# Optimization experiments

Measured on AMD Instinct MI355X. Metric: run time of the kernel, lower is better.

## Reference

```python
import jax, jax.numpy as jnp
import numpy as np

NBINS = (128, 64, 32)
MIN_BIN_WIDTH = 1e-3
MIN_BIN_HEIGHT = 1e-3


def quadratic_spline(inputs, unnorm_widths, unnorm_heights):
    """Piecewise-quadratic CDF spline (nflows-style). inputs: (N,) in [0,1],
    unnorm_widths: (N, nb), unnorm_heights: (N, nb+1). Returns (outputs, logabsdet)."""
    num_bins = unnorm_widths.shape[-1]
    widths = jax.nn.softmax(unnorm_widths, axis=-1)
    widths = MIN_BIN_WIDTH + (1.0 - MIN_BIN_WIDTH * num_bins) * widths
    hexp = jnp.exp(unnorm_heights)
    # normalize piecewise-linear pdf to integrate to 1
    area = jnp.sum(0.5 * (hexp[:, :-1] + hexp[:, 1:]) * widths, axis=-1, keepdims=True)
    heights = hexp / area
    heights = MIN_BIN_HEIGHT + (1.0 - MIN_BIN_HEIGHT) * heights
    bin_cdf = jnp.cumsum(0.5 * (heights[:, :-1] + heights[:, 1:]) * widths, axis=-1)
    bin_left_cdf = jnp.pad(bin_cdf.at[:, -1].set(1.0), ((0, 0), (1, 0)))
    bin_loc = jnp.cumsum(widths, axis=-1)
    bin_locations = jnp.pad(bin_loc.at[:, -1].set(1.0), ((0, 0), (1, 0)))
    bin_idx = jnp.clip(jnp.sum((inputs[:, None] >= bin_locations).astype(jnp.int32), axis=-1) - 1,
                       0, num_bins - 1)[:, None]
    take = lambda t, i: jnp.take_along_axis(t, i, axis=-1)[:, 0]
    loc = take(bin_locations, bin_idx)
    w = take(widths, bin_idx)
    cdf = take(bin_left_cdf, bin_idx)
    hl = take(heights, bin_idx)
    hr = take(heights, bin_idx + 1)
    alpha = (inputs - loc) / w
    outputs = jnp.clip(0.5 * (hr - hl) * w * alpha * alpha + hl * w * alpha + cdf, 0.0, 1.0)
    logabsdet = jnp.log(alpha * (hr - hl) + hl)
    return outputs, logabsdet


def _forward(coordinates, clustering, delta_height_weight, delta_baseline_weight,
             unnormalized_heights, unnormalized_widths, baseline_bias,
             genes_oi, local_gene_ix, local_cellxgene_ix, localcellxgene_ix):
    n_total_genes = delta_baseline_weight.shape[0]
    # decoder
    dhw = delta_height_weight[genes_oi]                            # (G, L, K)
    mixture_delta = jnp.einsum('cl,glk->cgk', clustering, dhw)     # (C, G, K)
    baseline_delta = clustering @ delta_baseline_weight.T          # (C, n_total)
    baseline = jax.nn.softmax(jnp.log(baseline_bias)[None, :] + baseline_delta, axis=-1)
    baseline_cuts = baseline.reshape(-1)[localcellxgene_ix]        # (N,)
    delta = mixture_delta.reshape(-1, mixture_delta.shape[-1])[local_cellxgene_ix]  # (N, K)
    gene_global = genes_oi[local_gene_ix]                          # (N,)
    # quadratic spline stack log_prob (base = Uniform[0,1])
    x = coordinates
    logabsdet = jnp.zeros_like(coordinates)
    ho = 0
    wo = 0
    for n in NBINS:
        uh = unnormalized_heights[:, ho:ho + n][gene_global] + delta[:, ho:ho + n]
        uw = unnormalized_widths[:, wo:wo + n - 1][gene_global]
        x, lad = quadratic_spline(x, uw, uh)
        logabsdet = logabsdet + lad
        ho += n
        wo += n - 1
    likelihood_position = logabsdet
    likelihood_region = jnp.log(baseline_cuts) + jnp.log(jnp.asarray(n_total_genes, jnp.float32))
    elbo = -(likelihood_position + likelihood_region).sum()
    # KL regularization (scales = exp(log 1.0) = 1)
    half_log_2pi = float(0.5 * np.log(2.0 * np.pi))
    mixture_kl = -0.5 * dhw * dhw - half_log_2pi
    baseline_kl = -0.5 * jnp.square(delta_baseline_weight[genes_oi]) - half_log_2pi
    return elbo - mixture_kl.sum() - baseline_kl.sum()


def setup_inputs() -> dict:
    key = jax.random.key(0)
    ks = jax.random.split(key, 10)
    N, C, G, NT, L = 500_000, 1000, 500, 10_000, 16
    K = sum(NBINS)                # 224 heights / delta components
    W = sum(n - 1 for n in NBINS)  # 221 widths
    coordinates = jax.random.uniform(ks[0], (N,), jnp.float32, 1e-4, 1.0 - 1e-4)
    cluster_id = jax.random.randint(ks[1], (C,), 0, L)
    clustering = jax.nn.one_hot(cluster_id, L, dtype=jnp.float32)
    genes_oi = jnp.sort(jax.random.permutation(ks[2], NT)[:G]).astype(jnp.int32)
    cell_ix = jax.random.randint(ks[3], (N,), 0, C)
    local_gene_ix = jax.random.randint(ks[4], (N,), 0, G).astype(jnp.int32)
    local_cellxgene_ix = (cell_ix * G + local_gene_ix).astype(jnp.int32)
    localcellxgene_ix = (cell_ix * NT + genes_oi[local_gene_ix]).astype(jnp.int32)
    delta_height_weight = jax.random.normal(ks[5], (NT, L, K), jnp.float32) * 0.05
    delta_baseline_weight = jax.random.uniform(ks[6], (NT, L), jnp.float32, -0.25, 0.25)
    unnormalized_heights = jax.random.normal(ks[7], (NT, K), jnp.float32) * 0.1
    unnormalized_widths = jax.random.normal(ks[8], (NT, W), jnp.float32) * 0.1
    baseline_bias = jax.random.uniform(ks[9], (NT,), jnp.float32, 1e-5, 1.0)
    return {
        'coordinates': coordinates, 'clustering': clustering,
        'delta_height_weight': delta_height_weight,
        'delta_baseline_weight': delta_baseline_weight,
        'unnormalized_heights': unnormalized_heights,
        'unnormalized_widths': unnormalized_widths,
        'baseline_bias': baseline_bias,
        'genes_oi': genes_oi, 'local_gene_ix': local_gene_ix,
        'local_cellxgene_ix': local_cellxgene_ix,
        'localcellxgene_ix': localcellxgene_ix,
    }


def reference(coordinates, clustering, delta_height_weight, delta_baseline_weight,
              unnormalized_heights, unnormalized_widths, baseline_bias,
              genes_oi, local_gene_ix, local_cellxgene_ix, localcellxgene_ix):
    return _forward(coordinates, clustering, delta_height_weight, delta_baseline_weight,
                    unnormalized_heights, unnormalized_widths, baseline_bias,
                    genes_oi, local_gene_ix, local_cellxgene_ix, localcellxgene_ix)
```

## Files before the change

kernel.cpp:

```cpp
#include <hip/hip_runtime.h>
#include <math.h>


#define CAP 192
static constexpr float  F_MBW = 1e-3f;
static constexpr float  F_MBH = 1e-3f;
static constexpr double D_HL2PI = 0.918938533204672741780329736406;


__global__ void __launch_bounds__(256)
kA(const float* __restrict__ clustering, int* __restrict__ cid,
   double* __restrict__ dpart, int* __restrict__ cnt, int C, int L, int P) {
  int bid = blockIdx.x, tid = threadIdx.x;
  if (bid < 4) {
    int c = bid * 256 + tid;
    if (c < C) {
      const float* row = clustering + (size_t)c * L;
      int best = 0; float bv = row[0];
      for (int l = 1; l < L; ++l) { float v = row[l]; if (v > bv) { bv = v; best = l; } }
      cid[c] = best;
    }
  } else {
    if (bid == 4 && tid < 128) dpart[tid] = 0.0;
    int i = (bid - 4) * 256 + tid;
    if (i < P) cnt[i] = 0;
  }
}

__global__ void __launch_bounds__(256)
kB(const float* __restrict__ coords, const int* __restrict__ lgi,
   const int* __restrict__ lcg, const int* __restrict__ cid,
   const float* __restrict__ bb, const float* __restrict__ dbw,
   int* __restrict__ cnt, float* __restrict__ xs, double* __restrict__ dpart,
   int N, int G, int L, int NT, int SCAT) {
  int bid = blockIdx.x;
  if (bid < SCAT) {
    int n0 = (bid * 256 + threadIdx.x) * 2;
    #pragma unroll
    for (int q = 0; q < 2; ++q) {
      int n = n0 + q;
      if (n < N) {
        int pair = lgi[n] * L + cid[lcg[n] / G];
        int pos = atomicAdd(&cnt[pair], 1);
        if (pos < CAP) xs[(size_t)pair * CAP + pos] = coords[n];
      }
    }
  } else {
    int g = (bid - SCAT) * 256 + threadIdx.x;
    float s[16];
    #pragma unroll
    for (int l = 0; l < 16; ++l) s[l] = 0.f;
    if (g < NT) {
      float b = bb[g];
      const float4* row = (const float4*)(dbw + (size_t)g * 16);
      #pragma unroll
      for (int q = 0; q < 4; ++q) {
        float4 v = row[q];
        s[4 * q + 0] = b * expf(v.x); s[4 * q + 1] = b * expf(v.y);
        s[4 * q + 2] = b * expf(v.z); s[4 * q + 3] = b * expf(v.w);
      }
    }
    __shared__ float partl[4][16];
    int lane = threadIdx.x & 63, wv = threadIdx.x >> 6;
    #pragma unroll
    for (int l = 0; l < 16; ++l) {
      float v = s[l];
      for (int off = 32; off; off >>= 1) v += __shfl_xor(v, off);
      if (lane == 0) partl[wv][l] = v;
    }
    __syncthreads();
    if (threadIdx.x < 16) {
      float t = partl[0][threadIdx.x] + partl[1][threadIdx.x]
              + partl[2][threadIdx.x] + partl[3][threadIdx.x];
      atomicAdd(&dpart[threadIdx.x * 8], (double)t);
    }
  }
}

static __device__ __forceinline__ float wscan(float v, int lane) {
  #pragma unroll
  for (int off = 1; off < 64; off <<= 1) {
    float u = __shfl_up(v, off, 64);
    if (lane >= off) v += u;
  }
  return v;
}

__global__ void __launch_bounds__(64)
k_pair(const float* __restrict__ uh, const float* __restrict__ uw,
       const float* __restrict__ dhw, const int* __restrict__ genes_oi,
       const float* __restrict__ xs, const int* __restrict__ cnt,
       const float* __restrict__ bb, const float* __restrict__ dbw,
       const double* __restrict__ dpart,
       float* __restrict__ partA, float* __restrict__ partB,
       int L, int K, int W, int NT) {
  int p = blockIdx.x;
  int g = p / L;
  int cl = p - g * L;
  int gg = genes_oi[g];
  const float* uhg  = uh + (size_t)gg * K;
  const float* uwg  = uw + (size_t)gg * W;
  const float* drow = dhw + ((size_t)gg * L + cl) * K;
  int t = threadIdx.x;

  __shared__ float4 tab[224];
  __shared__ int    grd[224];
  __shared__ float  s_h[128];

  const float cw128 = 1.0f - F_MBW * 127.0f;
  const float chh   = 1.0f - F_MBH;
  float d2;

  {
    int i0 = 2 * t, i1 = 2 * t + 1;
    float2 dv = *(const float2*)(drow + i0);
    float2 uv = *(const float2*)(uhg + i0);
    d2 = dv.x * dv.x + dv.y * dv.y;
    float hexp0 = expf(uv.x + dv.x), hexp1 = expf(uv.y + dv.y);
    s_h[i0] = hexp0; s_h[i1] = hexp1;
    float ew0 = expf(uwg[i0]);
    float ew1 = (i1 < 127) ? expf(uwg[i1]) : 0.f;
    float ps = wscan(ew0 + ew1, t);
    float wsum = __shfl(ps, 63);
    float incl0 = ps - ew1;
    float excl0 = incl0 - ew0, excl1 = incl0;
    float rw = cw128 / wsum;
    float width0 = F_MBW + rw * ew0;
    float width1 = F_MBW + rw * ew1;
    float loc0 = F_MBW * (float)i0 + rw * excl0;
    float loc1 = F_MBW * (float)i1 + rw * excl1;
    __syncthreads();
    float hn = (i1 < 127) ? s_h[i1 + 1] : 0.f;
    float at0 = 0.5f * (hexp0 + hexp1) * width0;
    float at1 = (i1 < 127) ? 0.5f * (hexp1 + hn) * width1 : 0.f;
    float pa = wscan(at0 + at1, t);
    float area = __shfl(pa, 63);
    float aincl0 = pa - at1;
    float aexcl0 = aincl0 - at0, aexcl1 = aincl0;
    float ra = chh / area;
    float h0 = F_MBH + ra * hexp0, h1 = F_MBH + ra * hexp1;
    float cdf0 = F_MBH * loc0 + ra * aexcl0;
    float cdf1 = F_MBH * loc1 + ra * aexcl1;
    if (i1 == 127) { loc1 = 1.0f; cdf1 = 1.0f; }
    tab[i0] = make_float4(loc0, cdf0, h0, 0.f);
    tab[i1] = make_float4(loc1, cdf1, h1, 0.f);
  }

  int ho = 128, wo = 127, tb = 128;
  #pragma unroll
  for (int lev = 1; lev < 3; ++lev) {
    const int nbp1 = (lev == 1) ? 64 : 32;
    const int nb = nbp1 - 1;
    const float cwl = 1.0f - F_MBW * (float)nb;
    float dvx = (t < nbp1) ? drow[ho + t] : 0.f;
    d2 += dvx * dvx;
    float hexp = (t < nbp1) ? expf(uhg[ho + t] + dvx) : 0.f;
    __syncthreads();
    s_h[t] = hexp;
    float ew = (t < nb) ? expf(uwg[wo + t]) : 0.f;
    float ips = wscan(ew, t);
    float wsum = __shfl(ips, nb - 1);
    float excl = ips - ew;
    float rw = cwl / wsum;
    float width = F_MBW + rw * ew;
    float loc = F_MBW * (float)t + rw * excl;
    __syncthreads();
    float hn = (t + 1 < nbp1) ? s_h[t + 1] : 0.f;
    float at = (t < nb) ? 0.5f * (hexp + hn) * width : 0.f;
    float ipa = wscan(at, t);
    float area = __shfl(ipa, nb - 1);
    float aexcl = ipa - at;
    float ra = chh / area;
    float h = F_MBH + ra * hexp;
    float cdf = F_MBH * loc + ra * aexcl;
    if (t == nb) { loc = 1.0f; cdf = 1.0f; }
    if (t < nbp1) tab[tb + t] = make_float4(loc, cdf, h, 0.f);
    ho += nbp1; wo += nb; tb += nbp1;
  }
  __syncthreads();

  {
    #pragma unroll
    for (int q = 0; q < 2; ++q) {
      int j = 2 * t + q;
      float target = (float)j * (1.0f / 128.0f);
      int lo = 0, hi = 128;
      #pragma unroll
      for (int it = 0; it < 7; ++it) {
        int mid = (lo + hi) >> 1;
        if (tab[mid].x <= target) lo = mid; else hi = mid;
      }
      grd[j] = (lo > 126) ? 126 : lo;
    }
    {
      float target = (float)t * (1.0f / 64.0f);
      int lo = 0, hi = 64;
      #pragma unroll
      for (int it = 0; it < 6; ++it) {
        int mid = (lo + hi) >> 1;
        if (tab[128 + mid].x <= target) lo = mid; else hi = mid;
      }
      grd[128 + t] = (lo > 62) ? 62 : lo;
    }
    if (t < 32) {
      float target = (float)t * (1.0f / 32.0f);
      int lo = 0, hi = 32;
      #pragma unroll
      for (int it = 0; it < 5; ++it) {
        int mid = (lo + hi) >> 1;
        if (tab[192 + mid].x <= target) lo = mid; else hi = mid;
      }
      grd[192 + t] = (lo > 30) ? 30 : lo;
    }
  }
  __syncthreads();

  int m = cnt[p]; if (m > CAP) m = CAP;
  float lad_sum = 0.f;
  for (int i = t; i < m; i += 64) {
    float x = xs[(size_t)p * CAP + i];
    float lad = 0.f;
    int b2 = 0;
    #pragma unroll
    for (int lev = 0; lev < 3; ++lev) {
      const int nbp1 = (lev == 0) ? 128 : (lev == 1) ? 64 : 32;
      int j = (int)(x * (float)nbp1);
      j = (j > nbp1 - 1) ? (nbp1 - 1) : j;
      int idx = grd[b2 + j];
      while (idx > 0 && tab[b2 + idx].x > x) --idx;
      while (idx < nbp1 - 2 && tab[b2 + idx + 1].x <= x) ++idx;
      float4 a = tab[b2 + idx];
      float4 b = tab[b2 + idx + 1];
      float w = b.x - a.x;
      float alpha = (x - a.x) / w;
      float dh = b.z - a.z;
      float outv = (0.5f * dh * alpha + a.z) * (w * alpha) + a.y;
      x = fminf(fmaxf(outv, 0.f), 1.f);
      lad += logf(alpha * dh + a.z);
      b2 += nbp1;
    }
    lad_sum += lad;
  }
  #pragma unroll
  for (int off = 32; off; off >>= 1) {
    lad_sum += __shfl_xor(lad_sum, off);
    d2      += __shfl_xor(d2, off);
  }
  if (t == 0) {
    float dv = dbw[(size_t)gg * L + cl];
    float rc = logf(bb[gg]) + dv - logf((float)dpart[cl * 8]) + logf((float)NT);
    partA[p] = lad_sum + (float)m * rc;
    partB[p] = d2 + dv * dv;
  }
}

__global__ void __launch_bounds__(256)
k_final(const float* __restrict__ partA, const float* __restrict__ partB,
        float* __restrict__ out, int P, long long M12) {
  int tid = threadIdx.x;
  double sa = 0.0, sb = 0.0;
  for (int i = tid; i < P; i += 256) { sa += (double)partA[i]; sb += (double)partB[i]; }
  __shared__ double rA[256], rB[256];
  rA[tid] = sa; rB[tid] = sb;
  __syncthreads();
  for (int off = 128; off > 0; off >>= 1) {
    if (tid < off) { rA[tid] += rA[tid + off]; rB[tid] += rB[tid + off]; }
    __syncthreads();
  }
  if (tid == 0)
    out[0] = (float)(-rA[0] + 0.5 * rB[0] + (double)M12 * D_HL2PI);
}

extern "C" void kernel_launch(void* const* d_in, const int* in_sizes, int n_in,
                              void* d_out, int out_size, void* d_ws, size_t ws_size,
                              hipStream_t stream) {
  const float* coords     = (const float*)d_in[0];
  const float* clustering = (const float*)d_in[1];
  const float* dhw        = (const float*)d_in[2];
  const float* dbw        = (const float*)d_in[3];
  const float* uh         = (const float*)d_in[4];
  const float* uw         = (const float*)d_in[5];
  const float* bb         = (const float*)d_in[6];
  const int*   genes_oi   = (const int*)d_in[7];
  const int*   lgi        = (const int*)d_in[8];
  const int*   lcg        = (const int*)d_in[9];

  int N  = in_sizes[0];
  int NT = in_sizes[6];
  int L  = in_sizes[3] / NT;
  int C  = in_sizes[1] / L;
  int K  = in_sizes[4] / NT;
  int W  = in_sizes[5] / NT;
  int G  = in_sizes[7];
  int P  = G * L;

  char* ws = (char*)d_ws;
  double* dpart = (double*)ws;
  int*    cid   = (int*)(ws + 4096);
  int*    cnt   = (int*)(ws + 8192);
  float*  partA = (float*)(ws + 40960);
  float*  partB = (float*)(ws + 73728);
  float*  xs    = (float*)(ws + 131072);

  int SCAT = (N + 511) / 512;
  int LSEB = (NT + 255) / 256;

  hipLaunchKernelGGL(kA, dim3(4 + (P + 255) / 256), dim3(256), 0, stream,
                     clustering, cid, dpart, cnt, C, L, P);
  hipLaunchKernelGGL(kB, dim3(SCAT + LSEB), dim3(256), 0, stream,
                     coords, lgi, lcg, cid, bb, dbw, cnt, xs, dpart,
                     N, G, L, NT, SCAT);
  hipLaunchKernelGGL(k_pair, dim3(P), dim3(64), 0, stream,
                     uh, uw, dhw, genes_oi, xs, cnt, bb, dbw, dpart,
                     partA, partB, L, K, W, NT);
  hipLaunchKernelGGL(k_final, dim3(1), dim3(256), 0, stream,
                     partA, partB, (float*)d_out, P,
                     (long long)G * L * K + (long long)G * L);
}
```

Baseline: 61.16 us.

## Fuse cluster argmax into scatter kernel, memset workspace, split spline table to SoA

Removes kernel kA. Each scatter block now recomputes the per-cell cluster argmax into shared memory, and the count and partial buffers are zeroed with hipMemsetAsync, which saves a kernel launch and the global cid round-trip. The per-pair spline table changes from float4 AoS to separate loc/cdf/height arrays, so the binary searches and bin walks read scalar loc values. The cost is redundant argmax work in every scatter block, and the s_cid buffer is only 1024 bytes, so it assumes C ≤ 1024 and L ≤ 256.

```diff
diff --git a/kernel.cpp b/kernel.cpp
--- a/kernel.cpp
+++ b/kernel.cpp
@@ -9,38 +9,27 @@
 
 
 __global__ void __launch_bounds__(256)
-kA(const float* __restrict__ clustering, int* __restrict__ cid,
-   double* __restrict__ dpart, int* __restrict__ cnt, int C, int L, int P) {
-  int bid = blockIdx.x, tid = threadIdx.x;
-  if (bid < 4) {
-    int c = bid * 256 + tid;
-    if (c < C) {
+kB(const float* __restrict__ coords, const int* __restrict__ lgi,
+   const int* __restrict__ lcg, const float* __restrict__ clustering,
+   const float* __restrict__ bb, const float* __restrict__ dbw,
+   int* __restrict__ cnt, float* __restrict__ xs, double* __restrict__ dpart,
+   int N, int C, int G, int L, int NT, int SCAT) {
+  int bid = blockIdx.x;
+  if (bid < SCAT) {
+    __shared__ unsigned char s_cid[1024];
+    for (int c = threadIdx.x; c < C; c += 256) {
       const float* row = clustering + (size_t)c * L;
       int best = 0; float bv = row[0];
       for (int l = 1; l < L; ++l) { float v = row[l]; if (v > bv) { bv = v; best = l; } }
-      cid[c] = best;
-    }
-  } else {
-    if (bid == 4 && tid < 128) dpart[tid] = 0.0;
-    int i = (bid - 4) * 256 + tid;
-    if (i < P) cnt[i] = 0;
-  }
-}
-
-__global__ void __launch_bounds__(256)
-kB(const float* __restrict__ coords, const int* __restrict__ lgi,
-   const int* __restrict__ lcg, const int* __restrict__ cid,
-   const float* __restrict__ bb, const float* __restrict__ dbw,
-   int* __restrict__ cnt, float* __restrict__ xs, double* __restrict__ dpart,
-   int N, int G, int L, int NT, int SCAT) {
-  int bid = blockIdx.x;
-  if (bid < SCAT) {
+      s_cid[c] = (unsigned char)best;
+    }
+    __syncthreads();
     int n0 = (bid * 256 + threadIdx.x) * 2;
     #pragma unroll
     for (int q = 0; q < 2; ++q) {
       int n = n0 + q;
       if (n < N) {
-        int pair = lgi[n] * L + cid[lcg[n] / G];
+        int pair = lgi[n] * L + (int)s_cid[lcg[n] / G];
         int pos = atomicAdd(&cnt[pair], 1);
         if (pos < CAP) xs[(size_t)pair * CAP + pos] = coords[n];
       }
@@ -103,9 +92,11 @@
   const float* drow = dhw + ((size_t)gg * L + cl) * K;
   int t = threadIdx.x;
 
-  __shared__ float4 tab[224];
-  __shared__ int    grd[224];
-  __shared__ float  s_h[128];
+  __shared__ float s_loc[224];
+  __shared__ float s_cdf[224];
+  __shared__ float s_hh[224];
+  __shared__ int   grd[224];
+  __shared__ float s_stg[128];
 
   const float cw128 = 1.0f - F_MBW * 127.0f;
   const float chh   = 1.0f - F_MBH;
@@ -117,7 +108,7 @@
     float2 uv = *(const float2*)(uhg + i0);
     d2 = dv.x * dv.x + dv.y * dv.y;
     float hexp0 = expf(uv.x + dv.x), hexp1 = expf(uv.y + dv.y);
-    s_h[i0] = hexp0; s_h[i1] = hexp1;
+    s_stg[i0] = hexp0; s_stg[i1] = hexp1;
     float ew0 = expf(uwg[i0]);
     float ew1 = (i1 < 127) ? expf(uwg[i1]) : 0.f;
     float ps = wscan(ew0 + ew1, t);
@@ -130,7 +121,7 @@
     float loc0 = F_MBW * (float)i0 + rw * excl0;
     float loc1 = F_MBW * (float)i1 + rw * excl1;
     __syncthreads();
-    float hn = (i1 < 127) ? s_h[i1 + 1] : 0.f;
+    float hn = (i1 < 127) ? s_stg[i1 + 1] : 0.f;
     float at0 = 0.5f * (hexp0 + hexp1) * width0;
     float at1 = (i1 < 127) ? 0.5f * (hexp1 + hn) * width1 : 0.f;
     float pa = wscan(at0 + at1, t);
@@ -142,8 +133,8 @@
     float cdf0 = F_MBH * loc0 + ra * aexcl0;
     float cdf1 = F_MBH * loc1 + ra * aexcl1;
     if (i1 == 127) { loc1 = 1.0f; cdf1 = 1.0f; }
-    tab[i0] = make_float4(loc0, cdf0, h0, 0.f);
-    tab[i1] = make_float4(loc1, cdf1, h1, 0.f);
+    s_loc[i0] = loc0; s_cdf[i0] = cdf0; s_hh[i0] = h0;
+    s_loc[i1] = loc1; s_cdf[i1] = cdf1; s_hh[i1] = h1;
   }
 
   int ho = 128, wo = 127, tb = 128;
@@ -156,7 +147,7 @@
     d2 += dvx * dvx;
     float hexp = (t < nbp1) ? expf(uhg[ho + t] + dvx) : 0.f;
     __syncthreads();
-    s_h[t] = hexp;
+    s_stg[t] = hexp;
     float ew = (t < nb) ? expf(uwg[wo + t]) : 0.f;
     float ips = wscan(ew, t);
     float wsum = __shfl(ips, nb - 1);
@@ -165,7 +156,7 @@
     float width = F_MBW + rw * ew;
     float loc = F_MBW * (float)t + rw * excl;
     __syncthreads();
-    float hn = (t + 1 < nbp1) ? s_h[t + 1] : 0.f;
+    float hn = (t + 1 < nbp1) ? s_stg[t + 1] : 0.f;
     float at = (t < nb) ? 0.5f * (hexp + hn) * width : 0.f;
     float ipa = wscan(at, t);
     float area = __shfl(ipa, nb - 1);
@@ -174,7 +165,7 @@
     float h = F_MBH + ra * hexp;
     float cdf = F_MBH * loc + ra * aexcl;
     if (t == nb) { loc = 1.0f; cdf = 1.0f; }
-    if (t < nbp1) tab[tb + t] = make_float4(loc, cdf, h, 0.f);
+    if (t < nbp1) { s_loc[tb + t] = loc; s_cdf[tb + t] = cdf; s_hh[tb + t] = h; }
     ho += nbp1; wo += nb; tb += nbp1;
   }
   __syncthreads();
@@ -188,7 +179,7 @@
       #pragma unroll
       for (int it = 0; it < 7; ++it) {
         int mid = (lo + hi) >> 1;
-        if (tab[mid].x <= target) lo = mid; else hi = mid;
+        if (s_loc[mid] <= target) lo = mid; else hi = mid;
       }
       grd[j] = (lo > 126) ? 126 : lo;
     }
@@ -198,7 +189,7 @@
       #pragma unroll
       for (int it = 0; it < 6; ++it) {
         int mid = (lo + hi) >> 1;
-        if (tab[128 + mid].x <= target) lo = mid; else hi = mid;
+        if (s_loc[128 + mid] <= target) lo = mid; else hi = mid;
       }
       grd[128 + t] = (lo > 62) ? 62 : lo;
     }
@@ -208,7 +199,7 @@
       #pragma unroll
       for (int it = 0; it < 5; ++it) {
         int mid = (lo + hi) >> 1;
-        if (tab[192 + mid].x <= target) lo = mid; else hi = mid;
+        if (s_loc[192 + mid] <= target) lo = mid; else hi = mid;
       }
       grd[192 + t] = (lo > 30) ? 30 : lo;
     }
@@ -227,16 +218,18 @@
       int j = (int)(x * (float)nbp1);
       j = (j > nbp1 - 1) ? (nbp1 - 1) : j;
       int idx = grd[b2 + j];
-      while (idx > 0 && tab[b2 + idx].x > x) --idx;
-      while (idx < nbp1 - 2 && tab[b2 + idx + 1].x <= x) ++idx;
-      float4 a = tab[b2 + idx];
-      float4 b = tab[b2 + idx + 1];
-      float w = b.x - a.x;
-      float alpha = (x - a.x) / w;
-      float dh = b.z - a.z;
-      float outv = (0.5f * dh * alpha + a.z) * (w * alpha) + a.y;
+      while (idx > 0 && s_loc[b2 + idx] > x) --idx;
+      while (idx < nbp1 - 2 && s_loc[b2 + idx + 1] <= x) ++idx;
+      float la = s_loc[b2 + idx];
+      float w  = s_loc[b2 + idx + 1] - la;
+      float cd = s_cdf[b2 + idx];
+      float hl = s_hh[b2 + idx];
+      float hr = s_hh[b2 + idx + 1];
+      float alpha = (x - la) / w;
+      float dh = hr - hl;
+      float outv = (0.5f * dh * alpha + hl) * (w * alpha) + cd;
       x = fminf(fmaxf(outv, 0.f), 1.f);
-      lad += logf(alpha * dh + a.z);
+      lad += logf(alpha * dh + hl);
       b2 += nbp1;
     }
     lad_sum += lad;
@@ -296,7 +289,6 @@
 
   char* ws = (char*)d_ws;
   double* dpart = (double*)ws;
-  int*    cid   = (int*)(ws + 4096);
   int*    cnt   = (int*)(ws + 8192);
   float*  partA = (float*)(ws + 40960);
   float*  partB = (float*)(ws + 73728);
@@ -305,11 +297,10 @@
   int SCAT = (N + 511) / 512;
   int LSEB = (NT + 255) / 256;
 
-  hipLaunchKernelGGL(kA, dim3(4 + (P + 255) / 256), dim3(256), 0, stream,
-                     clustering, cid, dpart, cnt, C, L, P);
+  hipMemsetAsync(ws, 0, 40960, stream);
   hipLaunchKernelGGL(kB, dim3(SCAT + LSEB), dim3(256), 0, stream,
-                     coords, lgi, lcg, cid, bb, dbw, cnt, xs, dpart,
-                     N, G, L, NT, SCAT);
+                     coords, lgi, lcg, clustering, bb, dbw, cnt, xs, dpart,
+                     N, C, G, L, NT, SCAT);
   hipLaunchKernelGGL(k_pair, dim3(P), dim3(64), 0, stream,
                      uh, uw, dhw, genes_oi, xs, cnt, bb, dbw, dpart,
                      partA, partB, L, K, W, NT);
```

Result: slower. 82.54 us (+34.9%).
